# Kernel tuning notes

Measured on AMD Instinct MI355X. Metric: run time of the kernel, lower is better.

The kernel has to match this reference:

```python
import jax, jax.numpy as jnp
import numpy as np
import math

B, S, D, H, L, DFF, V = 4, 1024, 512, 8, 4, 2048, 32000
DK = D // H
SPARSITY = 0.3
K = max(1, int(S * SPARSITY))  # 307
EPS = 1e-5


def _layernorm(x, g, b):
    mu = jnp.mean(x, axis=-1, keepdims=True)
    var = jnp.mean(jnp.square(x - mu), axis=-1, keepdims=True)
    return (x - mu) * jax.lax.rsqrt(var + EPS) * g + b


def _scatter_topk(scores, k):
    # scores: [B,H,S,S]. keep top-k per row, others -inf (torch.topk + scatter_)
    vals, idx = jax.lax.top_k(scores, k)
    lead = int(np.prod(scores.shape[:-1]))
    sk = scores.shape[-1]
    sparse = jnp.full((lead, sk), -jnp.inf, dtype=scores.dtype)
    rows = jnp.arange(lead)[:, None]
    sparse = sparse.at[rows, idx.reshape(lead, k)].set(vals.reshape(lead, k))
    return sparse.reshape(scores.shape)


def _forward(x, tok_emb, pos_emb, Wq, bq, Wk, bk, Wv, bv, Wo, bo,
             g1, be1, g2, be2, W1, b1, Wm, bm, W2, b2, Wout, bout):
    h = tok_emb[x] + pos_emb[jnp.arange(S)][None, :, :]  # [B,S,D]
    scale = 1.0 / math.sqrt(DK)
    for l in range(L):
        y = _layernorm(h, g1[l], be1[l])
        q = (y @ Wq[l] + bq[l]).reshape(B, S, H, DK).transpose(0, 2, 1, 3)
        kk = (y @ Wk[l] + bk[l]).reshape(B, S, H, DK).transpose(0, 2, 1, 3)
        v = (y @ Wv[l] + bv[l]).reshape(B, S, H, DK).transpose(0, 2, 1, 3)
        scores = jnp.einsum('bhqd,bhkd->bhqk', q, kk) * scale
        sparse = _scatter_topk(scores, K)
        attn = jax.nn.softmax(sparse, axis=-1)
        o = jnp.einsum('bhqk,bhkd->bhqd', attn, v)
        o = o.transpose(0, 2, 1, 3).reshape(B, S, D) @ Wo[l] + bo[l]
        h = h + o
        z = _layernorm(h, g2[l], be2[l])
        f = jax.nn.gelu(z @ W1[l] + b1[l], approximate=False)
        f = jax.nn.gelu(f @ Wm[l] + bm[l], approximate=False)
        f = f @ W2[l] + b2[l]
        h = h + f
    return h @ Wout + bout  # logits [B,S,V]


def setup_inputs() -> dict:
    key = jax.random.key(0)
    ks = iter(jax.random.split(key, 32))
    xa = lambda shape, fan: (jax.random.normal(next(ks), shape, jnp.float32)
                             * math.sqrt(2.0 / fan))
    return {
        'x': jax.random.randint(next(ks), (B, S), 0, V, dtype=jnp.int32),
        'tok_emb': xa((V, D), V + D),
        'pos_emb': xa((S, D), S + D),
        'Wq': xa((L, D, D), 2 * D), 'bq': jnp.zeros((L, D), jnp.float32),
        'Wk': xa((L, D, D), 2 * D), 'bk': jnp.zeros((L, D), jnp.float32),
        'Wv': xa((L, D, D), 2 * D), 'bv': jnp.zeros((L, D), jnp.float32),
        'Wo': xa((L, D, D), 2 * D), 'bo': jnp.zeros((L, D), jnp.float32),
        'g1': jnp.ones((L, D), jnp.float32), 'be1': jnp.zeros((L, D), jnp.float32),
        'g2': jnp.ones((L, D), jnp.float32), 'be2': jnp.zeros((L, D), jnp.float32),
        'W1': xa((L, D, DFF), D + DFF), 'b1': jnp.zeros((L, DFF), jnp.float32),
        'Wm': xa((L, DFF, DFF), 2 * DFF), 'bm': jnp.zeros((L, DFF), jnp.float32),
        'W2': xa((L, DFF, D), D + DFF), 'b2': jnp.zeros((L, D), jnp.float32),
        'Wout': xa((D, V), D + V), 'bout': jnp.zeros((V,), jnp.float32),
    }


def reference(x, tok_emb, pos_emb, Wq, bq, Wk, bk, Wv, bv, Wo, bo,
              g1, be1, g2, be2, W1, b1, Wm, bm, W2, b2, Wout, bout):
    return _forward(x, tok_emb, pos_emb, Wq, bq, Wk, bk, Wv, bv, Wo, bo,
                    g1, be1, g2, be2, W1, b1, Wm, bm, W2, b2, Wout, bout)
```

## Files before the change

### kernel.cpp

```cpp
#include <hip/hip_runtime.h>
#include <hip/hip_bf16.h>
#include <math.h>

#define B_ 4
#define S_ 1024
#define D_ 512
#define H_ 8
#define L_ 4
#define DFF_ 2048
#define V_ 32000
#define DK_ 64
#define KTOP 307
#define SRS 1048

using bf16x8 = __attribute__((ext_vector_type(8))) __bf16;
using bf16x4 = __attribute__((ext_vector_type(4))) __bf16;
using bf16x2 = __attribute__((ext_vector_type(2))) __bf16;
using f32x4v = __attribute__((ext_vector_type(4))) float;

__device__ __forceinline__ void gload_lds16(const __bf16* g, __bf16* l) {
  __builtin_amdgcn_global_load_lds(
      (const __attribute__((address_space(1))) void*)g,
      (__attribute__((address_space(3))) void*)l, 16, 0, 0);
}

__device__ __forceinline__ unsigned int f32_to_bf16_bits(float s) {
  unsigned int x = __float_as_uint(s);
  return (x + 0x7FFFu + ((x >> 16) & 1u)) >> 16;
}

__device__ __forceinline__ int red16i(int x) {
  x += __builtin_amdgcn_update_dpp(0, x, 0xB1, 0xF, 0xF, true);
  x += __builtin_amdgcn_update_dpp(0, x, 0x4E, 0xF, 0xF, true);
  x += __builtin_amdgcn_update_dpp(0, x, 0x141, 0xF, 0xF, true);
  x += __builtin_amdgcn_update_dpp(0, x, 0x140, 0xF, 0xF, true);
  return x;
}
__device__ __forceinline__ unsigned int red16umax(unsigned int x) {
  unsigned int t;
  t = (unsigned int)__builtin_amdgcn_update_dpp(0, (int)x, 0xB1, 0xF, 0xF, true);  x = t > x ? t : x;
  t = (unsigned int)__builtin_amdgcn_update_dpp(0, (int)x, 0x4E, 0xF, 0xF, true);  x = t > x ? t : x;
  t = (unsigned int)__builtin_amdgcn_update_dpp(0, (int)x, 0x141, 0xF, 0xF, true); x = t > x ? t : x;
  t = (unsigned int)__builtin_amdgcn_update_dpp(0, (int)x, 0x140, 0xF, 0xF, true); x = t > x ? t : x;
  return x;
}
__device__ __forceinline__ float red16f(float x) {
  x += __int_as_float(__builtin_amdgcn_update_dpp(0, __float_as_int(x), 0xB1, 0xF, 0xF, true));
  x += __int_as_float(__builtin_amdgcn_update_dpp(0, __float_as_int(x), 0x4E, 0xF, 0xF, true));
  x += __int_as_float(__builtin_amdgcn_update_dpp(0, __float_as_int(x), 0x141, 0xF, 0xF, true));
  x += __int_as_float(__builtin_amdgcn_update_dpp(0, __float_as_int(x), 0x140, 0xF, 0xF, true));
  return x;
}
__device__ __forceinline__ float red64f(float x) {
  x = red16f(x);
  x += __shfl_xor(x, 16, 64);
  x += __shfl_xor(x, 32, 64);
  return x;
}

template<int ROWS>
__device__ __forceinline__ void stage_tile4(const __bf16* src, int Kd, __bf16* lds,
                                            int w, int lane) {
  #pragma unroll
  for (int c = 0; c < ROWS / 32; ++c) {
    int rblk = (c * 4 + w) * 8;
    int row = rblk + (lane >> 3);
    int col = (lane & 7) * 8;
    int scol = col ^ ((row & 7) << 3);
    gload_lds16(src + (size_t)row * Kd + scol, lds + rblk * 64);
  }
}
__device__ __forceinline__ void stage_half8(const __bf16* src, int Kd, __bf16* lds,
                                            int w, int lane) {
  #pragma unroll
  for (int c = 0; c < 2; ++c) {
    int rblk = (c * 8 + w) * 8;
    int row = rblk + (lane >> 3);
    int col = (lane & 7) * 8;
    int scol = col ^ ((row & 7) << 3);
    gload_lds16(src + (size_t)row * Kd + scol, lds + rblk * 64);
  }
}
__device__ __forceinline__ bf16x8 lds_frag64(const __bf16* lds, int row, int colbase) {
  int col = colbase ^ ((row & 7) << 3);
  return *reinterpret_cast<const bf16x8*>(lds + row * 64 + col);
}

__global__ void embed_kernel(const int* __restrict__ x, const float* __restrict__ tok,
                             const float* __restrict__ pos, float* __restrict__ h) {
  int row = blockIdx.x;
  int t = threadIdx.x;
  int s = row & (S_ - 1);
  int token = x[row];
  const float4* t4 = reinterpret_cast<const float4*>(tok + (size_t)token * D_);
  const float4* p4 = reinterpret_cast<const float4*>(pos + (size_t)s * D_);
  float4 a = t4[t];
  float4 b = p4[t];
  a.x += b.x; a.y += b.y; a.z += b.z; a.w += b.w;
  reinterpret_cast<float4*>(h + (size_t)row * D_)[t] = a;
}

__global__ __launch_bounds__(256)
void ln_kernel(const float* __restrict__ xin, const float* __restrict__ g,
               const float* __restrict__ bta, __bf16* __restrict__ y) {
  int w = threadIdx.x >> 6, lane = threadIdx.x & 63;
  int row = blockIdx.x * 4 + w;
  const float4* x4 = reinterpret_cast<const float4*>(xin + (size_t)row * D_);
  float4 a = x4[lane * 2];
  float4 b = x4[lane * 2 + 1];
  float s = a.x + a.y + a.z + a.w + b.x + b.y + b.z + b.w;
  float q = a.x * a.x + a.y * a.y + a.z * a.z + a.w * a.w
          + b.x * b.x + b.y * b.y + b.z * b.z + b.w * b.w;
  s = red64f(s);
  q = red64f(q);
  float mu = s * (1.0f / D_);
  float var = q * (1.0f / D_) - mu * mu;
  float rstd = rsqrtf(var + 1e-5f);
  const float4* g4 = reinterpret_cast<const float4*>(g);
  const float4* b4 = reinterpret_cast<const float4*>(bta);
  float4 g0 = g4[lane * 2], g1 = g4[lane * 2 + 1];
  float4 e0 = b4[lane * 2], e1 = b4[lane * 2 + 1];
  bf16x8 o8;
  o8[0] = (__bf16)((a.x - mu) * rstd * g0.x + e0.x);
  o8[1] = (__bf16)((a.y - mu) * rstd * g0.y + e0.y);
  o8[2] = (__bf16)((a.z - mu) * rstd * g0.z + e0.z);
  o8[3] = (__bf16)((a.w - mu) * rstd * g0.w + e0.w);
  o8[4] = (__bf16)((b.x - mu) * rstd * g1.x + e1.x);
  o8[5] = (__bf16)((b.y - mu) * rstd * g1.y + e1.y);
  o8[6] = (__bf16)((b.z - mu) * rstd * g1.z + e1.z);
  o8[7] = (__bf16)((b.w - mu) * rstd * g1.w + e1.w);
  *reinterpret_cast<bf16x8*>(y + (size_t)row * D_ + lane * 8) = o8;
}

__global__ void transpose_bf16_kernel(const float* __restrict__ in, __bf16* __restrict__ out,
                                      int Kd, int N, long in_bstride, long out_bstride) {
  __shared__ float tile[32][33];
  const float* ib = in + (size_t)blockIdx.z * in_bstride;
  __bf16* ob = out + (size_t)blockIdx.z * out_bstride;
  int n0 = blockIdx.x * 32, k0 = blockIdx.y * 32;
  int tx = threadIdx.x & 31, ty = threadIdx.x >> 5;
  #pragma unroll
  for (int i = 0; i < 4; ++i)
    tile[ty + i * 8][tx] = ib[(size_t)(k0 + ty + i * 8) * N + n0 + tx];
  __syncthreads();
  #pragma unroll
  for (int i = 0; i < 4; ++i)
    ob[(size_t)(n0 + ty + i * 8) * Kd + k0 + tx] = (__bf16)tile[tx][ty + i * 8];
}

__global__ void concat_bias_kernel(const float* __restrict__ bq, const float* __restrict__ bk,
                                   const float* __restrict__ bv, float* __restrict__ bqkv) {
  int i = blockIdx.x * 256 + threadIdx.x;
  int l = i / 1536, c = i - l * 1536;
  float v = (c < 512) ? bq[l * 512 + c]
          : (c < 1024) ? bk[l * 512 + c - 512]
                       : bv[l * 512 + c - 1024];
  bqkv[i] = v;
}

#define BM 128
#define BN 128
#define BK 64

template<int OMODE, bool GELU_ACT, bool RES, bool SWZ>
__global__ __launch_bounds__(256)
void gemm_bf16_kernel(const __bf16* __restrict__ A, const __bf16* __restrict__ WT,
                      const float* __restrict__ bias, const float* __restrict__ res,
                      void* __restrict__ outp, void* __restrict__ outp2, void* __restrict__ outp3,
                      int M, int N, int Kd) {
  __shared__ __bf16 As[BM * BK];
  __shared__ __bf16 Ws[BN * BK];
  int tid = threadIdx.x;
  int lane = tid & 63, w = tid >> 6;
  int wr = w >> 1, wc = w & 1;
  int lr = lane & 15, lg = lane >> 4;
  int bx, by;
  if (SWZ) {
    int lid = blockIdx.x;
    int cpx = gridDim.x >> 3;
    int swz = (lid & 7) * cpx + (lid >> 3);
    int gx = M >> 7;
    bx = swz % gx;
    by = swz / gx;
  } else {
    bx = blockIdx.x; by = blockIdx.y;
  }
  int row0 = bx * BM, col0 = by * BN;

  const __bf16* Abase = A + (size_t)row0 * Kd;
  const __bf16* Wbase = WT + (size_t)col0 * Kd;

  f32x4v acc[4][4];
  #pragma unroll
  for (int i = 0; i < 4; ++i)
    #pragma unroll
    for (int j = 0; j < 4; ++j)
      #pragma unroll
      for (int e = 0; e < 4; ++e) acc[i][j][e] = 0.0f;

  for (int k0 = 0; k0 < Kd; k0 += BK) {
    stage_tile4<128>(Abase + k0, Kd, As, w, lane);
    stage_tile4<128>(Wbase + k0, Kd, Ws, w, lane);
    __syncthreads();
    bf16x8 af[4][2], bfr[4][2];
    #pragma unroll
    for (int mr = 0; mr < 4; ++mr)
      #pragma unroll
      for (int kk = 0; kk < 2; ++kk)
        af[mr][kk] = lds_frag64(As, wr * 64 + mr * 16 + lr, kk * 32 + lg * 8);
    #pragma unroll
    for (int nc = 0; nc < 4; ++nc)
      #pragma unroll
      for (int kk = 0; kk < 2; ++kk)
        bfr[nc][kk] = lds_frag64(Ws, wc * 64 + nc * 16 + lr, kk * 32 + lg * 8);
    __builtin_amdgcn_s_setprio(1);
    #pragma unroll
    for (int mr = 0; mr < 4; ++mr)
      #pragma unroll
      for (int nc = 0; nc < 4; ++nc) {
        acc[mr][nc] = __builtin_amdgcn_mfma_f32_16x16x32_bf16(af[mr][0], bfr[nc][0], acc[mr][nc], 0, 0, 0);
        acc[mr][nc] = __builtin_amdgcn_mfma_f32_16x16x32_bf16(af[mr][1], bfr[nc][1], acc[mr][nc], 0, 0, 0);
      }
    __builtin_amdgcn_s_setprio(0);
    __syncthreads();
  }

  #pragma unroll
  for (int mr = 0; mr < 4; ++mr) {
    #pragma unroll
    for (int nc = 0; nc < 4; ++nc) {
      int c = col0 + wc * 64 + nc * 16 + lr;
      int rb = row0 + wr * 64 + mr * 16 + lg * 4;
      float vv[4];
      #pragma unroll
      for (int j = 0; j < 4; ++j) {
        float t = acc[mr][nc][j] + bias[c];
        if (RES) t += res[(size_t)(rb + j) * N + c];
        if (GELU_ACT) t = 0.5f * t * (1.0f + erff(t * 0.70710678118654752f));
        vv[j] = t;
      }
      if (OMODE == 0) {
        float* out = (float*)outp;
        #pragma unroll
        for (int j = 0; j < 4; ++j) out[(size_t)(rb + j) * N + c] = vv[j];
      } else if (OMODE == 1) {
        __bf16* out = (__bf16*)outp;
        #pragma unroll
        for (int j = 0; j < 4; ++j) out[(size_t)(rb + j) * N + c] = (__bf16)vv[j];
      } else if (OMODE == 3) {
        float* out = (float*)outp;
        __bf16* out2 = (__bf16*)outp2;
        #pragma unroll
        for (int j = 0; j < 4; ++j) {
          out[(size_t)(rb + j) * N + c] = vv[j];
          out2[(size_t)(rb + j) * N + c] = (__bf16)vv[j];
        }
      }
    }
  }
}

template<int MTILE, int OMODE, bool GELU_ACT, bool RES>
__global__ __launch_bounds__(256)
void gemm_n128_kernel(const __bf16* __restrict__ A, const __bf16* __restrict__ WT,
                      const float* __restrict__ bias, const float* __restrict__ res,
                      void* __restrict__ outp, void* __restrict__ outp2, void* __restrict__ outp3,
                      int M, int N, int Kd) {
  constexpr int FR = MTILE / 32;
  __shared__ __bf16 As[MTILE * BK];
  __shared__ __bf16 Ws[BN * BK];
  int tid = threadIdx.x;
  int lane = tid & 63, w = tid >> 6;
  int wr = w >> 1, wc = w & 1;
  int lr = lane & 15, lg = lane >> 4;
  int row0 = blockIdx.x * MTILE, col0 = blockIdx.y * BN;

  const __bf16* Abase = A + (size_t)row0 * Kd;
  const __bf16* Wbase = WT + (size_t)col0 * Kd;

  f32x4v acc[FR][4];
  #pragma unroll
  for (int i = 0; i < FR; ++i)
    #pragma unroll
    for (int j = 0; j < 4; ++j)
      #pragma unroll
      for (int e = 0; e < 4; ++e) acc[i][j][e] = 0.0f;

  for (int k0 = 0; k0 < Kd; k0 += BK) {
    stage_tile4<MTILE>(Abase + k0, Kd, As, w, lane);
    stage_tile4<128>(Wbase + k0, Kd, Ws, w, lane);
    __syncthreads();
    bf16x8 af[FR][2], bfr[4][2];
    #pragma unroll
    for (int mr = 0; mr < FR; ++mr)
      #pragma unroll
      for (int kk = 0; kk < 2; ++kk)
        af[mr][kk] = lds_frag64(As, wr * (16 * FR) + mr * 16 + lr, kk * 32 + lg * 8);
    #pragma unroll
    for (int nc = 0; nc < 4; ++nc)
      #pragma unroll
      for (int kk = 0; kk < 2; ++kk)
        bfr[nc][kk] = lds_frag64(Ws, wc * 64 + nc * 16 + lr, kk * 32 + lg * 8);
    __builtin_amdgcn_s_setprio(1);
    #pragma unroll
    for (int mr = 0; mr < FR; ++mr)
      #pragma unroll
      for (int nc = 0; nc < 4; ++nc) {
        acc[mr][nc] = __builtin_amdgcn_mfma_f32_16x16x32_bf16(af[mr][0], bfr[nc][0], acc[mr][nc], 0, 0, 0);
        acc[mr][nc] = __builtin_amdgcn_mfma_f32_16x16x32_bf16(af[mr][1], bfr[nc][1], acc[mr][nc], 0, 0, 0);
      }
    __builtin_amdgcn_s_setprio(0);
    __syncthreads();
  }

  #pragma unroll
  for (int mr = 0; mr < FR; ++mr) {
    #pragma unroll
    for (int nc = 0; nc < 4; ++nc) {
      int c = col0 + wc * 64 + nc * 16 + lr;
      int rb = row0 + wr * (16 * FR) + mr * 16 + lg * 4;
      float vv[4];
      #pragma unroll
      for (int j = 0; j < 4; ++j) {
        float t = acc[mr][nc][j] + bias[c];
        if (RES) t += res[(size_t)(rb + j) * N + c];
        if (GELU_ACT) t = 0.5f * t * (1.0f + erff(t * 0.70710678118654752f));
        vv[j] = t;
      }
      if (OMODE == 0) {
        float* out = (float*)outp;
        #pragma unroll
        for (int j = 0; j < 4; ++j) out[(size_t)(rb + j) * N + c] = vv[j];
      } else if (OMODE == 1) {
        __bf16* out = (__bf16*)outp;
        #pragma unroll
        for (int j = 0; j < 4; ++j) out[(size_t)(rb + j) * N + c] = (__bf16)vv[j];
      } else if (OMODE == 3) {
        float* out = (float*)outp;
        __bf16* out2 = (__bf16*)outp2;
        #pragma unroll
        for (int j = 0; j < 4; ++j) {
          out[(size_t)(rb + j) * N + c] = vv[j];
          out2[(size_t)(rb + j) * N + c] = (__bf16)vv[j];
        }
      } else {
        if (col0 < 512) {
          __bf16* out = (__bf16*)outp;
          #pragma unroll
          for (int j = 0; j < 4; ++j) out[(size_t)(rb + j) * D_ + c] = (__bf16)vv[j];
        } else if (col0 < 1024) {
          __bf16* out = (__bf16*)outp2;
          #pragma unroll
          for (int j = 0; j < 4; ++j) out[(size_t)(rb + j) * D_ + (c - 512)] = (__bf16)vv[j];
        } else {
          __bf16* out = (__bf16*)outp3;
          int b = rb >> 10, s0 = rb & (S_ - 1);
          bf16x4 pk;
          #pragma unroll
          for (int j = 0; j < 4; ++j) pk[j] = (__bf16)vv[j];
          *reinterpret_cast<bf16x4*>(&out[((size_t)b * D_ + (c - 1024)) * S_ + s0]) = pk;
        }
      }
    }
  }
}

__global__ __launch_bounds__(512)
void gemm_head_kernel(const __bf16* __restrict__ A, const __bf16* __restrict__ WT,
                      const float* __restrict__ bias, float* __restrict__ out,
                      int M, int N, int Kd) {
  __shared__ __bf16 lds[2][2][256 * 64];
  const int tid = threadIdx.x;
  const int lane = tid & 63, w = tid >> 6;
  const int wr = w >> 2, wc = w & 3;
  const int lr = lane & 15, lg = lane >> 4;

  int lid = blockIdx.x;
  int cpx = gridDim.x >> 3;
  int swz = (lid & 7) * cpx + (lid >> 3);
  int gx = M >> 8;
  int bx = swz % gx, by = swz / gx;
  int row0 = bx * 256, col0 = by * 256;

  const __bf16* Asrc = A + (size_t)row0 * Kd;
  const __bf16* Bsrc = WT + (size_t)col0 * Kd;

  f32x4v acc[8][4];
  #pragma unroll
  for (int i = 0; i < 8; ++i)
    #pragma unroll
    for (int j = 0; j < 4; ++j)
      #pragma unroll
      for (int e = 0; e < 4; ++e) acc[i][j][e] = 0.0f;

  const int NT = Kd / 64;
  stage_half8(Asrc,                      Kd, &lds[0][0][0],    w, lane);
  stage_half8(Asrc + (size_t)128 * Kd,   Kd, &lds[0][0][8192], w, lane);
  stage_half8(Bsrc,                      Kd, &lds[0][1][0],    w, lane);
  stage_half8(Bsrc + (size_t)128 * Kd,   Kd, &lds[0][1][8192], w, lane);

  for (int t = 0; t < NT; ++t) {
    int cur = t & 1, nxt = cur ^ 1;
    int k1 = (t + 1) * 64;
    const __bf16* Ab = &lds[cur][0][0];
    const __bf16* Bb = &lds[cur][1][0];
    bf16x8 bfr[4][2];
    #pragma unroll
    for (int p = 0; p < 4; ++p) {
      if (t < NT - 1) {
        const __bf16* s;
        __bf16* d;
        if (p == 0)      { s = Asrc + k1;                    d = &lds[nxt][0][0]; }
        else if (p == 1) { s = Asrc + (size_t)128 * Kd + k1; d = &lds[nxt][0][8192]; }
        else if (p == 2) { s = Bsrc + k1;                    d = &lds[nxt][1][0]; }
        else             { s = Bsrc + (size_t)128 * Kd + k1; d = &lds[nxt][1][8192]; }
        stage_half8(s, Kd, d, w, lane);
      }
      if (p == 0) {
        if (t < NT - 1) asm volatile("s_waitcnt vmcnt(2)" ::: "memory");
        else            asm volatile("s_waitcnt vmcnt(0)" ::: "memory");
        __builtin_amdgcn_s_barrier();
        #pragma unroll
        for (int nn = 0; nn < 4; ++nn)
          #pragma unroll
          for (int kk = 0; kk < 2; ++kk)
            bfr[nn][kk] = lds_frag64(Bb, wc * 64 + nn * 16 + lr, kk * 32 + lg * 8);
      }
      bf16x8 af[2][2];
      #pragma unroll
      for (int mm = 0; mm < 2; ++mm)
        #pragma unroll
        for (int kk = 0; kk < 2; ++kk)
          af[mm][kk] = lds_frag64(Ab, wr * 128 + p * 32 + mm * 16 + lr, kk * 32 + lg * 8);
      asm volatile("s_waitcnt lgkmcnt(0)" ::: "memory");
      __builtin_amdgcn_sched_barrier(0);
      __builtin_amdgcn_s_setprio(1);
      #pragma unroll
      for (int mm = 0; mm < 2; ++mm)
        #pragma unroll
        for (int nn = 0; nn < 4; ++nn) {
          acc[p * 2 + mm][nn] = __builtin_amdgcn_mfma_f32_16x16x32_bf16(af[mm][0], bfr[nn][0], acc[p * 2 + mm][nn], 0, 0, 0);
          acc[p * 2 + mm][nn] = __builtin_amdgcn_mfma_f32_16x16x32_bf16(af[mm][1], bfr[nn][1], acc[p * 2 + mm][nn], 0, 0, 0);
        }
      __builtin_amdgcn_s_setprio(0);
    }
    __builtin_amdgcn_s_barrier();
  }

  #pragma unroll
  for (int mg = 0; mg < 8; ++mg) {
    #pragma unroll
    for (int nn = 0; nn < 4; ++nn) {
      int c = col0 + wc * 64 + nn * 16 + lr;
      int rb = row0 + wr * 128 + mg * 16 + lg * 4;
      float b = bias[c];
      #pragma unroll
      for (int j = 0; j < 4; ++j)
        out[(size_t)(rb + j) * N + c] = acc[mg][nn][j] + b;
    }
  }
}

__global__ __launch_bounds__(512)
void attn_kernel(const __bf16* __restrict__ qm, const __bf16* __restrict__ km,
                 const __bf16* __restrict__ vt, __bf16* __restrict__ o) {
  __shared__ unsigned short sc16[16][SRS];
  __shared__ float ored[4][64][4];
  __shared__ float rs[16];
  const int q0 = blockIdx.x * 16;
  const int hh = blockIdx.y;
  const int bb = blockIdx.z;
  const int tid = threadIdx.x;
  const int lane = tid & 63, w = tid >> 6;
  const int lr = lane & 15, lg = lane >> 4;

  const __bf16* qrow = qm + ((size_t)(bb * S_ + q0 + lr)) * D_ + hh * DK_;
  bf16x8 qf0 = *reinterpret_cast<const bf16x8*>(qrow + lg * 8);
  bf16x8 qf1 = *reinterpret_cast<const bf16x8*>(qrow + 32 + lg * 8);

  const __bf16* kbase = km + ((size_t)bb * S_) * D_ + hh * DK_;
  #pragma unroll
  for (int kt = 0; kt < 8; ++kt) {
    int key0 = kt * 128 + w * 16;
    const __bf16* krow = kbase + (size_t)(key0 + lr) * D_;
    bf16x8 kf0 = *reinterpret_cast<const bf16x8*>(krow + lg * 8);
    bf16x8 kf1 = *reinterpret_cast<const bf16x8*>(krow + 32 + lg * 8);
    f32x4v d = {0.0f, 0.0f, 0.0f, 0.0f};
    __builtin_amdgcn_s_setprio(1);
    d = __builtin_amdgcn_mfma_f32_16x16x32_bf16(qf0, kf0, d, 0, 0, 0);
    d = __builtin_amdgcn_mfma_f32_16x16x32_bf16(qf1, kf1, d, 0, 0, 0);
    __builtin_amdgcn_s_setprio(0);
    #pragma unroll
    for (int j = 0; j < 4; ++j) {
      unsigned int u = f32_to_bf16_bits(d[j] * 0.125f);
      u = (u & 0x8000u) ? (~u & 0xFFFFu) : (u | 0x8000u);
      sc16[lg * 4 + j][key0 + lr] = (unsigned short)u;
    }
  }
  __syncthreads();

  {
    int r = tid >> 5, tc = tid & 31;
    const unsigned int* srow = reinterpret_cast<const unsigned int*>(&sc16[r][0]);
    unsigned int wv[16];
    #pragma unroll
    for (int g = 0; g < 4; ++g) {
      uint4 t4 = *reinterpret_cast<const uint4*>(&srow[g * 128 + tc * 4]);
      wv[g * 4 + 0] = t4.x; wv[g * 4 + 1] = t4.y;
      wv[g * 4 + 2] = t4.z; wv[g * 4 + 3] = t4.w;
    }
    unsigned int umax = 0;
    #pragma unroll
    for (int i = 0; i < 16; ++i) {
      unsigned int a = wv[i] & 0xFFFFu, b = wv[i] >> 16;
      unsigned int mx = a > b ? a : b;
      umax = mx > umax ? mx : umax;
    }
    umax = red16umax(umax);
    {
      unsigned int other = (unsigned int)__shfl_xor((int)umax, 16, 32);
      umax = other > umax ? other : umax;
    }
    unsigned int lo = 0;
    for (int bit = 15; bit >= 0; --bit) {
      unsigned int cs = (lo | (1u << bit)) << 16;
      int cnt = 0;
      #pragma unroll
      for (int i = 0; i < 16; ++i) {
        cnt += ((wv[i] << 16) >= cs) ? 1 : 0;
        cnt += (wv[i] >= cs) ? 1 : 0;
      }
      cnt = red16i(cnt);
      cnt += __shfl_xor(cnt, 16, 32);
      if (cnt >= KTOP) lo |= (1u << bit);
    }
    unsigned int um = (umax & 0x8000u) ? (umax ^ 0x8000u) : (~umax & 0xFFFFu);
    float mval = __uint_as_float(um << 16);

    __bf16* P = reinterpret_cast<__bf16*>(&sc16[r][0]);
    float lsum = 0.0f;
    #pragma unroll
    for (int g = 0; g < 4; ++g) {
      bf16x8 pk;
      #pragma unroll
      for (int e = 0; e < 8; ++e) {
        unsigned int wrd = wv[g * 4 + (e >> 1)];
        unsigned int u = (e & 1) ? (wrd >> 16) : (wrd & 0xFFFFu);
        float p = 0.0f;
        if (u >= lo) {
          unsigned int ub = (u & 0x8000u) ? (u ^ 0x8000u) : (~u & 0xFFFFu);
          p = __expf(__uint_as_float(ub << 16) - mval);
        }
        pk[e] = (__bf16)p;
        lsum += (float)pk[e];
      }
      *reinterpret_cast<bf16x8*>(&P[tc * 8 + g * 256]) = pk;
    }
    lsum = red16f(lsum);
    lsum += __shfl_xor(lsum, 16, 32);
    if (tc == 0) rs[r] = 1.0f / lsum;
  }
  __syncthreads();

  {
    const __bf16* P0 = reinterpret_cast<const __bf16*>(&sc16[0][0]);
    int wc4 = w & 3;
    int half = w >> 2;
    const __bf16* vbase = vt + ((size_t)bb * D_ + hh * DK_ + wc4 * 16 + lr) * S_;
    const __bf16* prow = P0 + (size_t)lr * SRS;
    f32x4v oacc = {0.0f, 0.0f, 0.0f, 0.0f};
    int kt0 = half * 16;
    __builtin_amdgcn_s_setprio(1);
    #pragma unroll
    for (int kk = 0; kk < 16; ++kk) {
      int kt = kt0 + kk;
      bf16x8 a = *reinterpret_cast<const bf16x8*>(prow + kt * 32 + lg * 8);
      bf16x8 b = *reinterpret_cast<const bf16x8*>(vbase + kt * 32 + lg * 8);
      oacc = __builtin_amdgcn_mfma_f32_16x16x32_bf16(a, b, oacc, 0, 0, 0);
    }
    __builtin_amdgcn_s_setprio(0);
    if (half == 1) {
      float4 st;
      st.x = oacc[0]; st.y = oacc[1]; st.z = oacc[2]; st.w = oacc[3];
      *reinterpret_cast<float4*>(&ored[wc4][lane][0]) = st;
    }
    __syncthreads();
    if (half == 0) {
      float4 pv = *reinterpret_cast<const float4*>(&ored[wc4][lane][0]);
      oacc[0] += pv.x; oacc[1] += pv.y; oacc[2] += pv.z; oacc[3] += pv.w;
      #pragma unroll
      for (int j = 0; j < 4; ++j) {
        int qr = lg * 4 + j;
        float ov = oacc[j] * rs[qr];
        o[((size_t)(bb * S_ + q0 + qr)) * D_ + hh * DK_ + wc4 * 16 + lr] = (__bf16)ov;
      }
    }
  }
}

extern "C" void kernel_launch(void* const* d_in, const int* in_sizes, int n_in,
                              void* d_out, int out_size, void* d_ws, size_t ws_size,
                              hipStream_t stream) {
  (void)in_sizes; (void)n_in; (void)out_size; (void)ws_size;
  const int*   x    = (const int*)d_in[0];
  const float* tok  = (const float*)d_in[1];
  const float* pos  = (const float*)d_in[2];
  const float* Wq   = (const float*)d_in[3];
  const float* bq   = (const float*)d_in[4];
  const float* Wk   = (const float*)d_in[5];
  const float* bk   = (const float*)d_in[6];
  const float* Wv   = (const float*)d_in[7];
  const float* bv   = (const float*)d_in[8];
  const float* Wo   = (const float*)d_in[9];
  const float* bo   = (const float*)d_in[10];
  const float* g1   = (const float*)d_in[11];
  const float* be1  = (const float*)d_in[12];
  const float* g2   = (const float*)d_in[13];
  const float* be2  = (const float*)d_in[14];
  const float* W1   = (const float*)d_in[15];
  const float* b1   = (const float*)d_in[16];
  const float* Wm   = (const float*)d_in[17];
  const float* bm   = (const float*)d_in[18];
  const float* W2   = (const float*)d_in[19];
  const float* b2   = (const float*)d_in[20];
  const float* Wout = (const float*)d_in[21];
  const float* bout = (const float*)d_in[22];
  float* logits = (float*)d_out;

  const int M = B_ * S_;
  float* ws = (float*)d_ws;
  float* h    = ws;
  float* bqkv = h + (size_t)M * D_;
  __bf16* y16  = (__bf16*)(bqkv + (size_t)L_ * 1536);
  __bf16* f1b  = y16  + (size_t)M * D_;
  __bf16* f2b  = f1b  + (size_t)M * DFF_;
  __bf16* qb16 = f2b  + (size_t)M * DFF_;
  __bf16* kb16 = qb16 + (size_t)M * D_;
  __bf16* vt16 = kb16 + (size_t)M * D_;
  __bf16* ob16 = vt16 + (size_t)M * D_;
  __bf16* h16  = ob16 + (size_t)M * D_;
  __bf16* WqkvT = h16 + (size_t)M * D_;
  __bf16* WoT  = WqkvT + (size_t)L_ * 1536 * D_;
  __bf16* W1T  = WoT  + (size_t)L_ * D_ * D_;
  __bf16* WmT  = W1T  + (size_t)L_ * D_ * DFF_;
  __bf16* W2T  = WmT  + (size_t)L_ * DFF_ * DFF_;
  __bf16* WoutT = W2T + (size_t)L_ * D_ * DFF_;

  const long DD = (long)D_ * D_;
  transpose_bf16_kernel<<<dim3(D_/32,  D_/32,   L_), 256, 0, stream>>>(Wq, WqkvT,            D_, D_, DD, 1536L*D_);
  transpose_bf16_kernel<<<dim3(D_/32,  D_/32,   L_), 256, 0, stream>>>(Wk, WqkvT + 512*512,  D_, D_, DD, 1536L*D_);
  transpose_bf16_kernel<<<dim3(D_/32,  D_/32,   L_), 256, 0, stream>>>(Wv, WqkvT + 1024*512, D_, D_, DD, 1536L*D_);
  transpose_bf16_kernel<<<dim3(D_/32,  D_/32,   L_), 256, 0, stream>>>(Wo, WoT, D_, D_, DD, DD);
  transpose_bf16_kernel<<<dim3(DFF_/32, D_/32,  L_), 256, 0, stream>>>(W1, W1T, D_, DFF_, (long)D_*DFF_, (long)D_*DFF_);
  transpose_bf16_kernel<<<dim3(DFF_/32, DFF_/32,L_), 256, 0, stream>>>(Wm, WmT, DFF_, DFF_, (long)DFF_*DFF_, (long)DFF_*DFF_);
  transpose_bf16_kernel<<<dim3(D_/32,  DFF_/32, L_), 256, 0, stream>>>(W2, W2T, DFF_, D_, (long)D_*DFF_, (long)D_*DFF_);
  transpose_bf16_kernel<<<dim3(V_/32,  D_/32,   1 ), 256, 0, stream>>>(Wout, WoutT, D_, V_, (long)D_*V_, (long)D_*V_);
  concat_bias_kernel<<<(L_*1536)/256, 256, 0, stream>>>(bq, bk, bv, bqkv);

  embed_kernel<<<M, 128, 0, stream>>>(x, tok, pos, h);

  for (int l = 0; l < L_; ++l) {
    ln_kernel<<<M/4, 256, 0, stream>>>(h, g1 + l * D_, be1 + l * D_, y16);
    gemm_n128_kernel<64,4,false,false><<<dim3(M/64, 1536/BN), 256, 0, stream>>>(
        y16, WqkvT + (size_t)l * 1536 * D_, bqkv + l * 1536, nullptr,
        qb16, kb16, vt16, M, 1536, D_);
    attn_kernel<<<dim3(S_/16, H_, B_), 512, 0, stream>>>(qb16, kb16, vt16, ob16);
    gemm_n128_kernel<32,0,false,true><<<dim3(M/32, D_/BN), 256, 0, stream>>>(
        ob16, WoT + (size_t)l * DD, bo + l * D_, h, h, nullptr, nullptr, M, D_, D_);
    ln_kernel<<<M/4, 256, 0, stream>>>(h, g2 + l * D_, be2 + l * D_, y16);
    gemm_n128_kernel<64,1,true,false><<<dim3(M/64, DFF_/BN), 256, 0, stream>>>(
        y16, W1T + (size_t)l * D_ * DFF_, b1 + l * DFF_, nullptr, f1b, nullptr, nullptr, M, DFF_, D_);
    gemm_bf16_kernel<1,true,false,true><<<dim3((M/BM) * (DFF_/BN)), 256, 0, stream>>>(
        f1b, WmT + (size_t)l * DFF_ * DFF_, bm + l * DFF_, nullptr, f2b, nullptr, nullptr, M, DFF_, DFF_);
    gemm_n128_kernel<32,3,false,true><<<dim3(M/32, D_/BN), 256, 0, stream>>>(
        f2b, W2T + (size_t)l * D_ * DFF_, b2 + l * D_, h, h, h16, nullptr, M, D_, DFF_);
  }
  gemm_head_kernel<<<dim3((M/256) * (V_/256)), 512, 0, stream>>>(
      h16, WoutT, bout, logits, M, V_, D_);
}
```

Before: 1.170 ms.

## Batch weight transposes into one launch and XCD-swizzle n128 GEMM grids

Merges the eight per-matrix weight transpose launches into a single batched kernel driven by a job table passed by value, so there are fewer launches and fewer small partial waves. It also flattens the grids of the gemm_n128 kernels to 1D and remaps block IDs with an XCD-aware swizzle, so tiles that share A or W rows are placed on the same chiplet for L2 reuse. The swizzle assumes the grid size divides evenly by 8, and the batched transpose adds a per-block job lookup loop.

```diff
diff --git a/kernel.cpp b/kernel.cpp
--- a/kernel.cpp
+++ b/kernel.cpp
@@ -84,6 +84,11 @@
 __device__ __forceinline__ bf16x8 lds_frag64(const __bf16* lds, int row, int colbase) {
   int col = colbase ^ ((row & 7) << 3);
   return *reinterpret_cast<const bf16x8*>(lds + row * 64 + col);
+}
+
+__device__ __forceinline__ int xcd_swz(int lid, int nwg) {
+  int cpx = nwg >> 3;
+  return (lid & 7) * cpx + (lid >> 3);
 }
 
 __global__ void embed_kernel(const int* __restrict__ x, const float* __restrict__ tok,
@@ -132,20 +137,43 @@
   *reinterpret_cast<bf16x8*>(y + (size_t)row * D_ + lane * 8) = o8;
 }
 
-__global__ void transpose_bf16_kernel(const float* __restrict__ in, __bf16* __restrict__ out,
-                                      int Kd, int N, long in_bstride, long out_bstride) {
-  __shared__ float tile[32][33];
-  const float* ib = in + (size_t)blockIdx.z * in_bstride;
-  __bf16* ob = out + (size_t)blockIdx.z * out_bstride;
-  int n0 = blockIdx.x * 32, k0 = blockIdx.y * 32;
-  int tx = threadIdx.x & 31, ty = threadIdx.x >> 5;
-  #pragma unroll
-  for (int i = 0; i < 4; ++i)
-    tile[ty + i * 8][tx] = ib[(size_t)(k0 + ty + i * 8) * N + n0 + tx];
-  __syncthreads();
-  #pragma unroll
-  for (int i = 0; i < 4; ++i)
-    ob[(size_t)(n0 + ty + i * 8) * Kd + k0 + tx] = (__bf16)tile[tx][ty + i * 8];
+struct TJob {
+  const float* src;
+  __bf16* dst;
+  int Kd, N, nx, ny;
+  long ibs, obs;
+  int base, cnt;
+};
+struct TJobs { TJob j[8]; };
+
+__global__ __launch_bounds__(256)
+void transpose_batch_kernel(TJobs jobs) {
+  int bid = blockIdx.x;
+  #pragma unroll
+  for (int d = 0; d < 8; ++d) {
+    const TJob& J = jobs.j[d];
+    if (bid >= J.base && bid < J.base + J.cnt) {
+      int lid = bid - J.base;
+      int pz = J.nx * J.ny;
+      int z = lid / pz;
+      int rem = lid - z * pz;
+      int y = rem / J.nx;
+      int x = rem - y * J.nx;
+      __shared__ float tile[32][33];
+      const float* ib = J.src + (size_t)z * J.ibs;
+      __bf16* ob = J.dst + (size_t)z * J.obs;
+      int n0 = x * 32, k0 = y * 32;
+      int tx = threadIdx.x & 31, ty = threadIdx.x >> 5;
+      #pragma unroll
+      for (int i = 0; i < 4; ++i)
+        tile[ty + i * 8][tx] = ib[(size_t)(k0 + ty + i * 8) * J.N + n0 + tx];
+      __syncthreads();
+      #pragma unroll
+      for (int i = 0; i < 4; ++i)
+        ob[(size_t)(n0 + ty + i * 8) * J.Kd + k0 + tx] = (__bf16)tile[tx][ty + i * 8];
+      return;
+    }
+  }
 }
 
 __global__ void concat_bias_kernel(const float* __restrict__ bq, const float* __restrict__ bk,
@@ -176,9 +204,7 @@
   int lr = lane & 15, lg = lane >> 4;
   int bx, by;
   if (SWZ) {
-    int lid = blockIdx.x;
-    int cpx = gridDim.x >> 3;
-    int swz = (lid & 7) * cpx + (lid >> 3);
+    int swz = xcd_swz(blockIdx.x, gridDim.x);
     int gx = M >> 7;
     bx = swz % gx;
     by = swz / gx;
@@ -273,7 +299,10 @@
   int lane = tid & 63, w = tid >> 6;
   int wr = w >> 1, wc = w & 1;
   int lr = lane & 15, lg = lane >> 4;
-  int row0 = blockIdx.x * MTILE, col0 = blockIdx.y * BN;
+  int swz = xcd_swz(blockIdx.x, gridDim.x);
+  int gx = M / MTILE;
+  int bx = swz % gx, by = swz / gx;
+  int row0 = bx * MTILE, col0 = by * BN;
 
   const __bf16* Abase = A + (size_t)row0 * Kd;
   const __bf16* Wbase = WT + (size_t)col0 * Kd;
@@ -375,9 +404,7 @@
   const int wr = w >> 2, wc = w & 3;
   const int lr = lane & 15, lg = lane >> 4;
 
-  int lid = blockIdx.x;
-  int cpx = gridDim.x >> 3;
-  int swz = (lid & 7) * cpx + (lid >> 3);
+  int swz = xcd_swz(blockIdx.x, gridDim.x);
   int gx = M >> 8;
   int bx = swz % gx, by = swz / gx;
   int row0 = bx * 256, col0 = by * 256;
@@ -646,33 +673,44 @@
   __bf16* W2T  = WmT  + (size_t)L_ * DFF_ * DFF_;
   __bf16* WoutT = W2T + (size_t)L_ * D_ * DFF_;
 
+  TJobs tj;
+  int base = 0;
+  auto addjob = [&](int idx, const float* src, __bf16* dst, int Kd, int N,
+                    long ibs, long obs, int nz) {
+    TJob& J = tj.j[idx];
+    J.src = src; J.dst = dst; J.Kd = Kd; J.N = N;
+    J.nx = N / 32; J.ny = Kd / 32; J.ibs = ibs; J.obs = obs;
+    J.base = base; J.cnt = J.nx * J.ny * nz;
+    base += J.cnt;
+  };
   const long DD = (long)D_ * D_;
-  transpose_bf16_kernel<<<dim3(D_/32,  D_/32,   L_), 256, 0, stream>>>(Wq, WqkvT,            D_, D_, DD, 1536L*D_);
-  transpose_bf16_kernel<<<dim3(D_/32,  D_/32,   L_), 256, 0, stream>>>(Wk, WqkvT + 512*512,  D_, D_, DD, 1536L*D_);
-  transpose_bf16_kernel<<<dim3(D_/32,  D_/32,   L_), 256, 0, stream>>>(Wv, WqkvT + 1024*512, D_, D_, DD, 1536L*D_);
-  transpose_bf16_kernel<<<dim3(D_/32,  D_/32,   L_), 256, 0, stream>>>(Wo, WoT, D_, D_, DD, DD);
-  transpose_bf16_kernel<<<dim3(DFF_/32, D_/32,  L_), 256, 0, stream>>>(W1, W1T, D_, DFF_, (long)D_*DFF_, (long)D_*DFF_);
-  transpose_bf16_kernel<<<dim3(DFF_/32, DFF_/32,L_), 256, 0, stream>>>(Wm, WmT, DFF_, DFF_, (long)DFF_*DFF_, (long)DFF_*DFF_);
-  transpose_bf16_kernel<<<dim3(D_/32,  DFF_/32, L_), 256, 0, stream>>>(W2, W2T, DFF_, D_, (long)D_*DFF_, (long)D_*DFF_);
-  transpose_bf16_kernel<<<dim3(V_/32,  D_/32,   1 ), 256, 0, stream>>>(Wout, WoutT, D_, V_, (long)D_*V_, (long)D_*V_);
+  addjob(0, Wq,   WqkvT,            D_,   D_,   DD, 1536L * D_, L_);
+  addjob(1, Wk,   WqkvT + 512*512,  D_,   D_,   DD, 1536L * D_, L_);
+  addjob(2, Wv,   WqkvT + 1024*512, D_,   D_,   DD, 1536L * D_, L_);
+  addjob(3, Wo,   WoT,              D_,   D_,   DD, DD,          L_);
+  addjob(4, W1,   W1T,              D_,   DFF_, (long)D_*DFF_, (long)D_*DFF_, L_);
+  addjob(5, Wm,   WmT,              DFF_, DFF_, (long)DFF_*DFF_, (long)DFF_*DFF_, L_);
+  addjob(6, W2,   W2T,              DFF_, D_,   (long)D_*DFF_, (long)D_*DFF_, L_);
+  addjob(7, Wout, WoutT,            D_,   V_,   (long)D_*V_,   (long)D_*V_,   1);
+  transpose_batch_kernel<<<base, 256, 0, stream>>>(tj);
+
   concat_bias_kernel<<<(L_*1536)/256, 256, 0, stream>>>(bq, bk, bv, bqkv);
-
   embed_kernel<<<M, 128, 0, stream>>>(x, tok, pos, h);
 
   for (int l = 0; l < L_; ++l) {
     ln_kernel<<<M/4, 256, 0, stream>>>(h, g1 + l * D_, be1 + l * D_, y16);
-    gemm_n128_kernel<64,4,false,false><<<dim3(M/64, 1536/BN), 256, 0, stream>>>(
+    gemm_n128_kernel<64,4,false,false><<<dim3((M/64) * (1536/BN)), 256, 0, stream>>>(
         y16, WqkvT + (size_t)l * 1536 * D_, bqkv + l * 1536, nullptr,
         qb16, kb16, vt16, M, 1536, D_);
     attn_kernel<<<dim3(S_/16, H_, B_), 512, 0, stream>>>(qb16, kb16, vt16, ob16);
-    gemm_n128_kernel<32,0,false,true><<<dim3(M/32, D_/BN), 256, 0, stream>>>(
+    gemm_n128_kernel<32,0,false,true><<<dim3((M/32) * (D_/BN)), 256, 0, stream>>>(
         ob16, WoT + (size_t)l * DD, bo + l * D_, h, h, nullptr, nullptr, M, D_, D_);
     ln_kernel<<<M/4, 256, 0, stream>>>(h, g2 + l * D_, be2 + l * D_, y16);
-    gemm_n128_kernel<64,1,true,false><<<dim3(M/64, DFF_/BN), 256, 0, stream>>>(
+    gemm_n128_kernel<64,1,true,false><<<dim3((M/64) * (DFF_/BN)), 256, 0, stream>>>(
         y16, W1T + (size_t)l * D_ * DFF_, b1 + l * DFF_, nullptr, f1b, nullptr, nullptr, M, DFF_, D_);
     gemm_bf16_kernel<1,true,false,true><<<dim3((M/BM) * (DFF_/BN)), 256, 0, stream>>>(
         f1b, WmT + (size_t)l * DFF_ * DFF_, bm + l * DFF_, nullptr, f2b, nullptr, nullptr, M, DFF_, DFF_);
-    gemm_n128_kernel<32,3,false,true><<<dim3(M/32, D_/BN), 256, 0, stream>>>(
+    gemm_n128_kernel<32,3,false,true><<<dim3((M/32) * (D_/BN)), 256, 0, stream>>>(
         f2b, W2T + (size_t)l * D_ * DFF_, b2 + l * D_, h, h, h16, nullptr, M, D_, DFF_);
   }
   gemm_head_kernel<<<dim3((M/256) * (V_/256)), 512, 0, stream>>>(
```

New measurement: 1.167 ms. About the same (-0.3%).
